# Performance work log

Measured on AMD Instinct MI355X. Metric: run time of the kernel, lower is better.

## Reference

```python
import jax, jax.numpy as jnp
import numpy as np

B, S, V, CTX, NC, D, NH, L, FF, MAXS = 8, 512, 32000, 8, 512, 256, 4, 4, 512, 512
PAD = 0  # ram_model.pad_token_id


def setup_inputs() -> dict:
    key = jax.random.key(0)
    ks = iter(jax.random.split(key, 64))
    def p(shape, s=0.02):
        return jax.random.normal(next(ks), shape, jnp.float32) * s
    inp = {}
    inp["token_ids"] = jax.random.randint(next(ks), (B, S), 0, V)
    inp["ram_table"] = p((V, NC), 0.1)          # frozen RAM per-cluster scores
    inp["proj_W"] = p((NC, D)); inp["proj_b"] = jnp.zeros((D,), jnp.float32)
    inp["pos_emb"] = p((MAXS, D))
    for pre in ("sa", "ca"):
        for nm in ("Wq", "Wk", "Wv", "Wo"):
            inp[f"{pre}_{nm}"] = p((L, D, D))
        for nm in ("bq", "bk", "bv", "bo"):
            inp[f"{pre}_{nm}"] = jnp.zeros((L, D), jnp.float32)
    for i in (1, 2, 3):
        inp[f"ln{i}_s"] = jnp.ones((L, D), jnp.float32)
        inp[f"ln{i}_b"] = jnp.zeros((L, D), jnp.float32)
    inp["ff_W1"] = p((L, D, FF)); inp["ff_b1"] = jnp.zeros((L, FF), jnp.float32)
    inp["ff_W2"] = p((L, FF, D)); inp["ff_b2"] = jnp.zeros((L, D), jnp.float32)
    inp["out_W"] = p((D, V)); inp["out_b"] = jnp.zeros((V,), jnp.float32)
    return inp


def _ln(x, s, b):
    m = x.mean(-1, keepdims=True)
    v = ((x - m) ** 2).mean(-1, keepdims=True)
    return (x - m) * jax.lax.rsqrt(v + 1e-5) * s + b


def _mha(q_in, k_in, v_in, Wq, bq, Wk, bk, Wv, bv, Wo, bo, mask):
    b, sq, d = q_in.shape
    hd = d // NH
    q = (q_in @ Wq + bq).reshape(b, sq, NH, hd)
    k = (k_in @ Wk + bk).reshape(b, -1, NH, hd)
    v = (v_in @ Wv + bv).reshape(b, -1, NH, hd)
    sc = jnp.einsum("bqhd,bkhd->bhqk", q, k) / np.sqrt(hd).astype(np.float32)
    if mask is not None:
        sc = jnp.where(mask, -1e9, sc)  # mask broadcast over [b, h]
    a = jax.nn.softmax(sc, axis=-1)
    o = jnp.einsum("bhqk,bkhd->bqhd", a, v).reshape(b, sq, d)
    return o @ Wo + bo


def _forward(token_ids, ram_table, proj_W, proj_b, pos_emb,
             sa_Wq, sa_bq, sa_Wk, sa_bk, sa_Wv, sa_bv, sa_Wo, sa_bo,
             ca_Wq, ca_bq, ca_Wk, ca_bk, ca_Wv, ca_bv, ca_Wo, ca_bo,
             ln1_s, ln1_b, ln2_s, ln2_b, ln3_s, ln3_b,
             ff_W1, ff_b1, ff_W2, ff_b2, out_W, out_b):
    b, s = token_ids.shape
    # Batched sliding context windows (replaces the per-position Python loop):
    # left-pad with PAD so window at pos covers [pos-CTX+1, pos].
    padded = jnp.concatenate(
        [jnp.full((b, CTX - 1), PAD, token_ids.dtype), token_ids], axis=1)
    idx = jnp.arange(s)[:, None] + jnp.arange(CTX)[None, :]  # [S, CTX]
    win = padded[:, idx]                                      # [B, S, CTX]
    # Frozen RAM feature extraction: per-cluster scores averaged over window.
    scores = ram_table[win].mean(axis=2)                      # [B, S, NC]
    x = scores @ proj_W + proj_b + pos_emb[:s]                # [B, S, D]
    mask = jnp.triu(jnp.ones((s, s), bool), 1)                # causal
    mem = jnp.zeros((b, 1, D), x.dtype)
    for l in range(L):
        h = _ln(x, ln1_s[l], ln1_b[l])
        x = x + _mha(h, h, h, sa_Wq[l], sa_bq[l], sa_Wk[l], sa_bk[l],
                     sa_Wv[l], sa_bv[l], sa_Wo[l], sa_bo[l], mask)
        h = _ln(x, ln2_s[l], ln2_b[l])
        x = x + _mha(h, mem, mem, ca_Wq[l], ca_bq[l], ca_Wk[l], ca_bk[l],
                     ca_Wv[l], ca_bv[l], ca_Wo[l], ca_bo[l], None)
        h = _ln(x, ln3_s[l], ln3_b[l])
        x = x + jax.nn.relu(h @ ff_W1[l] + ff_b1[l]) @ ff_W2[l] + ff_b2[l]
    return x @ out_W + out_b                                  # [B, S, V]


def reference(token_ids, ram_table, proj_W, proj_b, pos_emb,
              sa_Wq, sa_bq, sa_Wk, sa_bk, sa_Wv, sa_bv, sa_Wo, sa_bo,
              ca_Wq, ca_bq, ca_Wk, ca_bk, ca_Wv, ca_bv, ca_Wo, ca_bo,
              ln1_s, ln1_b, ln2_s, ln2_b, ln3_s, ln3_b,
              ff_W1, ff_b1, ff_W2, ff_b2, out_W, out_b):
    return _forward(token_ids, ram_table, proj_W, proj_b, pos_emb,
                    sa_Wq, sa_bq, sa_Wk, sa_bk, sa_Wv, sa_bv, sa_Wo, sa_bo,
                    ca_Wq, ca_bq, ca_Wk, ca_bk, ca_Wv, ca_bv, ca_Wo, ca_bo,
                    ln1_s, ln1_b, ln2_s, ln2_b, ln3_s, ln3_b,
                    ff_W1, ff_b1, ff_W2, ff_b2, out_W, out_b)
```

## Files before the change

### kernel.cpp

```cpp
#include <hip/hip_runtime.h>

#define B_   8
#define S_   512
#define V_   32000
#define CTX_ 8
#define NC_  512
#define D_   256
#define NH_  4
#define L_   4
#define FF_  512
#define HD_  64
#define BS_  4096

#define FG_F32   1
#define FG_BF16  2
#define FG_RELU  4
#define FG_POS   8
#define FG_NT    16
#define FG_QKV   32

typedef __attribute__((ext_vector_type(8))) short bf16x8;
typedef __attribute__((ext_vector_type(4))) float f32x4;

__device__ inline void gload16(const void* g, void* lds) {
    __builtin_amdgcn_global_load_lds(
        (const __attribute__((address_space(1))) void*)g,
        (__attribute__((address_space(3))) void*)lds, 16, 0, 0);
}

__device__ inline ushort f2b(float f) {
    union { float f; unsigned u; } v; v.f = f;
    unsigned u = v.u;
    unsigned r = u + 0x7fffu + ((u >> 16) & 1u);
    return (ushort)(r >> 16);
}

__global__ __launch_bounds__(256) void prologue_kernel(
    const int* __restrict__ tok, const float* __restrict__ ram,
    const float* __restrict__ proj_W, const float* __restrict__ Wq,
    const float* __restrict__ Wk, const float* __restrict__ Wv,
    const float* __restrict__ Wo, const float* __restrict__ W1,
    const float* __restrict__ W2, const float* __restrict__ outW,
    const float* __restrict__ ca_bv, const float* __restrict__ ca_Wo,
    const float* __restrict__ ca_bo, const float* __restrict__ bq,
    const float* __restrict__ bk, const float* __restrict__ bv,
    ushort* __restrict__ pjWb, ushort* __restrict__ WqkvB,
    ushort* __restrict__ WoB, ushort* __restrict__ ff1B,
    ushort* __restrict__ ff2B, ushort* __restrict__ Wb,
    float* __restrict__ cc, float* __restrict__ qkvb,
    ushort* __restrict__ scores)
{
    __shared__ float tile[32 * 33];
    int id = blockIdx.x;
    int t = threadIdx.x;
    if (id < 10176) {
        const float* src; ushort* dst; int K, N, lt;
        if (id < 128)       { src = proj_W; dst = pjWb; K = 512; N = 256; lt = id; }
        else if (id < 896)  { lt = id - 128; int z = lt >> 6; lt &= 63;
                              int which = z / L_, l = z % L_;
                              src = (which == 0 ? Wq : which == 1 ? Wk : Wv) + (size_t)l * 65536;
                              dst = WqkvB + ((size_t)l * 768 + which * 256) * 256;
                              K = 256; N = 256; }
        else if (id < 1152) { lt = id - 896; int l = lt >> 6; lt &= 63;
                              src = Wo + (size_t)l * 65536; dst = WoB + (size_t)l * 65536;
                              K = 256; N = 256; }
        else if (id < 1664) { lt = id - 1152; int l = lt >> 7; lt &= 127;
                              src = W1 + (size_t)l * 131072; dst = ff1B + (size_t)l * 131072;
                              K = 256; N = 512; }
        else if (id < 2176) { lt = id - 1664; int l = lt >> 7; lt &= 127;
                              src = W2 + (size_t)l * 131072; dst = ff2B + (size_t)l * 131072;
                              K = 512; N = 256; }
        else                { lt = id - 2176; src = outW; dst = Wb; K = 256; N = 32000; }
        int ntc = N >> 5;
        int n0 = (lt % ntc) * 32, k0 = (lt / ntc) * 32;
        int tx = t & 31, ty = t >> 5;
        for (int i = ty; i < 32; i += 8)
            tile[i * 33 + tx] = src[(size_t)(k0 + i) * N + n0 + tx];
        __syncthreads();
        for (int i = ty; i < 32; i += 8)
            dst[(size_t)(n0 + i) * K + k0 + tx] = f2b(tile[tx * 33 + i]);
    } else if (id < 10180) {
        int l = id - 10176;
        const float* w = ca_Wo + (size_t)l * D_ * D_;
        const float* b = ca_bv + l * D_;
        float acc = 0.f;
        for (int d = 0; d < D_; ++d) acc += b[d] * w[(size_t)d * D_ + t];
        cc[l * D_ + t] = acc + ca_bo[l * D_ + t];
        for (int u = t; u < 768; u += 256) {
            int which = u >> 8, c = u & 255;
            const float* src = which == 0 ? bq : which == 1 ? bk : bv;
            qkvb[l * 768 + u] = src[l * 256 + c];
        }
    } else {
        int bs = id - 10180;
        int b = bs >> 9, s = bs & 511;
        float a0 = 0.f, a1 = 0.f;
        #pragma unroll
        for (int c = 0; c < CTX_; ++c) {
            int pos = s + c - (CTX_ - 1);
            int tk = (pos < 0) ? 0 : tok[b * S_ + pos];
            const float* row = ram + (size_t)tk * NC_;
            a0 += row[t];
            a1 += row[t + 256];
        }
        scores[(size_t)bs * NC_ + t]       = f2b(a0 * 0.125f);
        scores[(size_t)bs * NC_ + t + 256] = f2b(a1 * 0.125f);
    }
}

template<int K, int FLAGS>
__global__ __launch_bounds__(256) void gemm_row(
    const ushort* __restrict__ A, const ushort* __restrict__ Bt,
    const float* __restrict__ bias, const float* __restrict__ extra,
    const float* __restrict__ resid, const float* __restrict__ pos,
    const float* __restrict__ lnS, const float* __restrict__ lnB,
    float* __restrict__ Xout, ushort* __restrict__ Hout)
{
    __shared__ ushort As[16 * 64];
    __shared__ ushort Bs[256 * 64];
    __shared__ float red[2][4][16];
    int mt = blockIdx.x;
    int row0 = mt * 16;
    int t = threadIdx.x, w = t >> 6, lane = t & 63;
    int srow = lane >> 3, slot = lane & 7;
    int gcol = (slot ^ srow) * 8;
    int sl = lane >> 4, lc = lane & 15;
    int rA = lane & 15;

    f32x4 acc[4] = {};

    #pragma unroll
    for (int k0 = 0; k0 < K; k0 += 64) {
        if (w < 2)
            gload16(A + (size_t)(row0 + w * 8 + srow) * K + k0 + gcol, As + w * 512);
        #pragma unroll
        for (int c = 0; c < 8; ++c) {
            int chunk = w * 8 + c;
            gload16(Bt + (size_t)(chunk * 8 + srow) * K + k0 + gcol, Bs + chunk * 512);
        }
        __syncthreads();
        #pragma unroll
        for (int kk = 0; kk < 2; ++kk) {
            bf16x8 a = *reinterpret_cast<const bf16x8*>(
                As + rA * 64 + (((sl + kk * 4) ^ (rA & 7)) * 8));
            #pragma unroll
            for (int n = 0; n < 4; ++n) {
                int rr = w * 64 + (lane & 15) + n * 16;
                bf16x8 b = *reinterpret_cast<const bf16x8*>(
                    Bs + rr * 64 + (((sl + kk * 4) ^ (rr & 7)) * 8));
                acc[n] = __builtin_amdgcn_mfma_f32_16x16x32_bf16(a, b, acc[n], 0, 0, 0);
            }
        }
        __syncthreads();
    }

    float v[4][4];
    float psum[4] = {}, psq[4] = {};
    #pragma unroll
    for (int n = 0; n < 4; ++n) {
        int col = w * 64 + n * 16 + lc;
        float bn = bias[col];
        float en = extra ? extra[col] : 0.f;
        #pragma unroll
        for (int r = 0; r < 4; ++r) {
            int row = row0 + sl * 4 + r;
            float x = acc[n][r] + bn;
            if constexpr (FLAGS & FG_POS) x += pos[(size_t)(row & 511) * D_ + col];
            x += en;
            if (resid) x += resid[(size_t)row * D_ + col];
            v[n][r] = x;
            psum[r] += x;
            psq[r] += x * x;
        }
    }
    #pragma unroll
    for (int r = 0; r < 4; ++r) {
        #pragma unroll
        for (int o = 8; o > 0; o >>= 1) {
            psum[r] += __shfl_xor(psum[r], o);
            psq[r]  += __shfl_xor(psq[r], o);
        }
    }
    if (lc == 0) {
        #pragma unroll
        for (int r = 0; r < 4; ++r) {
            red[0][w][sl * 4 + r] = psum[r];
            red[1][w][sl * 4 + r] = psq[r];
        }
    }
    __syncthreads();
    #pragma unroll
    for (int r = 0; r < 4; ++r) {
        int rl = sl * 4 + r;
        float s  = red[0][0][rl] + red[0][1][rl] + red[0][2][rl] + red[0][3][rl];
        float s2 = red[1][0][rl] + red[1][1][rl] + red[1][2][rl] + red[1][3][rl];
        float mean = s * (1.f / D_);
        float var = s2 * (1.f / D_) - mean * mean;
        float rstd = rsqrtf(var + 1e-5f);
        int row = row0 + rl;
        #pragma unroll
        for (int n = 0; n < 4; ++n) {
            int col = w * 64 + n * 16 + lc;
            float x = v[n][r];
            Xout[(size_t)row * D_ + col] = x;
            Hout[(size_t)row * D_ + col] =
                f2b((x - mean) * rstd * lnS[col] + lnB[col]);
        }
    }
}

template<bool LAST>
__global__ __launch_bounds__(256) void tail_fused_kernel(
    const ushort* __restrict__ pv, const ushort* __restrict__ WoT,
    const float* __restrict__ bo, const float* __restrict__ ccl,
    const float* __restrict__ xin,
    const float* __restrict__ ln3S, const float* __restrict__ ln3B,
    const ushort* __restrict__ W1t, const ushort* __restrict__ W2t,
    const float* __restrict__ b1, const float* __restrict__ b2,
    const float* __restrict__ ln1S, const float* __restrict__ ln1B,
    float* __restrict__ Xout, ushort* __restrict__ Hout,
    ushort* __restrict__ XBout)
{
    __shared__ ushort Ah[16 * 256];
    __shared__ ushort As1[16 * 64];
    __shared__ ushort Bs1[64 * 256];
    __shared__ ushort Bs2[256 * 64];
    __shared__ ushort As2[16 * 64];
    __shared__ float red[2][4][16];
    int row0 = blockIdx.x * 16;
    int t = threadIdx.x, w = t >> 6, lane = t & 63;
    int srow = lane >> 3, slot = lane & 7;
    int gcol = (slot ^ srow) * 8;
    int sl = lane >> 4, lc = lane & 15;
    int rA = lane & 15;

    f32x4 acc[4] = {};
    #pragma unroll
    for (int k0 = 0; k0 < 256; k0 += 64) {
        if (w < 2)
            gload16(pv + (size_t)(row0 + w * 8 + srow) * 256 + k0 + gcol, As1 + w * 512);
        #pragma unroll
        for (int c = 0; c < 8; ++c) {
            int chunk = w * 8 + c;
            gload16(WoT + (size_t)(chunk * 8 + srow) * 256 + k0 + gcol, Bs2 + chunk * 512);
        }
        __syncthreads();
        #pragma unroll
        for (int kk = 0; kk < 2; ++kk) {
            bf16x8 a = *reinterpret_cast<const bf16x8*>(
                As1 + rA * 64 + (((sl + kk * 4) ^ (rA & 7)) * 8));
            #pragma unroll
            for (int n = 0; n < 4; ++n) {
                int rr = w * 64 + rA + n * 16;
                bf16x8 b = *reinterpret_cast<const bf16x8*>(
                    Bs2 + rr * 64 + (((sl + kk * 4) ^ (rr & 7)) * 8));
                acc[n] = __builtin_amdgcn_mfma_f32_16x16x32_bf16(a, b, acc[n], 0, 0, 0);
            }
        }
        __syncthreads();
    }

    float v[4][4];
    {
        float psum[4] = {}, psq[4] = {};
        #pragma unroll
        for (int n = 0; n < 4; ++n) {
            int col = w * 64 + n * 16 + lc;
            float bn = bo[col] + ccl[col];
            #pragma unroll
            for (int r = 0; r < 4; ++r) {
                int row = row0 + sl * 4 + r;
                float x = acc[n][r] + bn + xin[(size_t)row * D_ + col];
                v[n][r] = x;
                psum[r] += x;
                psq[r] += x * x;
            }
        }
        #pragma unroll
        for (int r = 0; r < 4; ++r) {
            #pragma unroll
            for (int o = 8; o > 0; o >>= 1) {
                psum[r] += __shfl_xor(psum[r], o);
                psq[r]  += __shfl_xor(psq[r], o);
            }
        }
        if (lc == 0) {
            #pragma unroll
            for (int r = 0; r < 4; ++r) {
                red[0][w][sl * 4 + r] = psum[r];
                red[1][w][sl * 4 + r] = psq[r];
            }
        }
        __syncthreads();
        #pragma unroll
        for (int r = 0; r < 4; ++r) {
            int rl = sl * 4 + r;
            float s  = red[0][0][rl] + red[0][1][rl] + red[0][2][rl] + red[0][3][rl];
            float s2 = red[1][0][rl] + red[1][1][rl] + red[1][2][rl] + red[1][3][rl];
            float mean = s * (1.f / D_);
            float var = s2 * (1.f / D_) - mean * mean;
            float rstd = rsqrtf(var + 1e-5f);
            #pragma unroll
            for (int n = 0; n < 4; ++n) {
                int col = w * 64 + n * 16 + lc;
                int colk = n * 16 + lc;
                float h = (v[n][r] - mean) * rstd * ln3S[col] + ln3B[col];
                Ah[w * 1024 + rl * 64 + (((colk >> 3) ^ (rl & 7)) * 8) + (colk & 7)] =
                    f2b(h);
            }
        }
    }
    __syncthreads();

    f32x4 xacc[4] = {};
    for (int c8 = 0; c8 < 8; ++c8) {
        int f0 = c8 * 64;
        #pragma unroll
        for (int c = 0; c < 8; ++c) {
            int chunk = w * 8 + c;
            int ks = chunk >> 3, rg = chunk & 7;
            gload16(W1t + (size_t)(f0 + rg * 8 + srow) * 256 + ks * 64 + gcol,
                    Bs1 + chunk * 512);
        }
        #pragma unroll
        for (int c = 0; c < 8; ++c) {
            int chunk = w * 8 + c;
            gload16(W2t + (size_t)(chunk * 8 + srow) * 512 + f0 + gcol,
                    Bs2 + chunk * 512);
        }
        __syncthreads();

        f32x4 a2 = {};
        #pragma unroll
        for (int ks = 0; ks < 4; ++ks) {
            #pragma unroll
            for (int kk = 0; kk < 2; ++kk) {
                bf16x8 a = *reinterpret_cast<const bf16x8*>(
                    Ah + ks * 1024 + rA * 64 + (((sl + kk * 4) ^ (rA & 7)) * 8));
                int rB = w * 16 + rA;
                bf16x8 b = *reinterpret_cast<const bf16x8*>(
                    Bs1 + ks * 4096 + rB * 64 + (((sl + kk * 4) ^ (rB & 7)) * 8));
                a2 = __builtin_amdgcn_mfma_f32_16x16x32_bf16(a, b, a2, 0, 0, 0);
            }
        }
        {
            float bn = b1[f0 + w * 16 + lc];
            #pragma unroll
            for (int r = 0; r < 4; ++r) {
                float p = fmaxf(a2[r] + bn, 0.f);
                int prow = sl * 4 + r;
                int pcol = w * 16 + lc;
                As2[prow * 64 + (((pcol >> 3) ^ (prow & 7)) * 8) + (pcol & 7)] = f2b(p);
            }
        }
        __syncthreads();
        #pragma unroll
        for (int kk = 0; kk < 2; ++kk) {
            bf16x8 a = *reinterpret_cast<const bf16x8*>(
                As2 + rA * 64 + (((sl + kk * 4) ^ (rA & 7)) * 8));
            #pragma unroll
            for (int n = 0; n < 4; ++n) {
                int rB = w * 64 + n * 16 + rA;
                bf16x8 b = *reinterpret_cast<const bf16x8*>(
                    Bs2 + rB * 64 + (((sl + kk * 4) ^ (rB & 7)) * 8));
                xacc[n] = __builtin_amdgcn_mfma_f32_16x16x32_bf16(a, b, xacc[n], 0, 0, 0);
            }
        }
        __syncthreads();
    }

    float psum[4] = {}, psq[4] = {};
    #pragma unroll
    for (int n = 0; n < 4; ++n) {
        int col = w * 64 + n * 16 + lc;
        float bn = b2[col];
        #pragma unroll
        for (int r = 0; r < 4; ++r) {
            float x = xacc[n][r] + bn + v[n][r];
            v[n][r] = x;
            psum[r] += x;
            psq[r] += x * x;
        }
    }
    if constexpr (LAST) {
        #pragma unroll
        for (int n = 0; n < 4; ++n) {
            int col = w * 64 + n * 16 + lc;
            #pragma unroll
            for (int r = 0; r < 4; ++r) {
                int row = row0 + sl * 4 + r;
                XBout[(size_t)row * D_ + col] = f2b(v[n][r]);
            }
        }
        return;
    }
    #pragma unroll
    for (int r = 0; r < 4; ++r) {
        #pragma unroll
        for (int o = 8; o > 0; o >>= 1) {
            psum[r] += __shfl_xor(psum[r], o);
            psq[r]  += __shfl_xor(psq[r], o);
        }
    }
    if (lc == 0) {
        #pragma unroll
        for (int r = 0; r < 4; ++r) {
            red[0][w][sl * 4 + r] = psum[r];
            red[1][w][sl * 4 + r] = psq[r];
        }
    }
    __syncthreads();
    #pragma unroll
    for (int r = 0; r < 4; ++r) {
        int rl = sl * 4 + r;
        float s  = red[0][0][rl] + red[0][1][rl] + red[0][2][rl] + red[0][3][rl];
        float s2 = red[1][0][rl] + red[1][1][rl] + red[1][2][rl] + red[1][3][rl];
        float mean = s * (1.f / D_);
        float var = s2 * (1.f / D_) - mean * mean;
        float rstd = rsqrtf(var + 1e-5f);
        int row = row0 + rl;
        #pragma unroll
        for (int n = 0; n < 4; ++n) {
            int col = w * 64 + n * 16 + lc;
            float x = v[n][r];
            Xout[(size_t)row * D_ + col] = x;
            Hout[(size_t)row * D_ + col] =
                f2b((x - mean) * rstd * ln1S[col] + ln1B[col]);
        }
    }
}

template<int BM, int BN, int K, int TN, int FLAGS>
__global__ __launch_bounds__(256) void gemm_t(
    const ushort* __restrict__ A, const ushort* __restrict__ Bt,
    const float* __restrict__ bias, const float* __restrict__ extra,
    const float* __restrict__ resid, const float* __restrict__ pos,
    float* __restrict__ Cf, ushort* __restrict__ Cb)
{
    constexpr int WM = BM / 32;
    constexpr int WN = BN / 32;
    constexpr int MT = 4096 / BM;
    constexpr int NWG = MT * (TN / BN);
    __shared__ ushort smem[(BM + BN) * 64];
    ushort* As = smem;
    ushort* Bs = smem + BM * 64;
    int bid = blockIdx.x;
    int swz = bid;
    if constexpr ((NWG & 7) == 0) {
        constexpr int cpx = NWG >> 3;
        swz = (bid & 7) * cpx + (bid >> 3);
    }
    int mt = swz % MT, nt = swz / MT;
    int row0 = mt * BM, col0 = nt * BN;
    int t = threadIdx.x, w = t >> 6, lane = t & 63;
    int wr = w >> 1, wc = w & 1;
    int srow = lane >> 3, slot = lane & 7;
    int gcol = (slot ^ srow) * 8;

    f32x4 acc[WM][WN] = {};
    int sl = lane >> 4;
    int rA0 = wr * (BM / 2) + (lane & 15);
    int rB0 = wc * (BN / 2) + (lane & 15);

    #pragma unroll
    for (int k0 = 0; k0 < K; k0 += 64) {
        #pragma unroll
        for (int c = 0; c < BM / 32; ++c) {
            int chunk = w * (BM / 32) + c;
            gload16(A + (size_t)(row0 + chunk * 8 + srow) * K + k0 + gcol,
                    As + chunk * 512);
        }
        #pragma unroll
        for (int c = 0; c < BN / 32; ++c) {
            int chunk = w * (BN / 32) + c;
            gload16(Bt + (size_t)(col0 + chunk * 8 + srow) * K + k0 + gcol,
                    Bs + chunk * 512);
        }
        __syncthreads();
        #pragma unroll
        for (int kk = 0; kk < 2; ++kk) {
            bf16x8 a[WM], b[WN];
            #pragma unroll
            for (int m = 0; m < WM; ++m) {
                int rr = rA0 + m * 16;
                a[m] = *reinterpret_cast<const bf16x8*>(
                    As + rr * 64 + (((sl + kk * 4) ^ (rr & 7)) * 8));
            }
            #pragma unroll
            for (int n = 0; n < WN; ++n) {
                int rr = rB0 + n * 16;
                b[n] = *reinterpret_cast<const bf16x8*>(
                    Bs + rr * 64 + (((sl + kk * 4) ^ (rr & 7)) * 8));
            }
            #pragma unroll
            for (int m = 0; m < WM; ++m)
                #pragma unroll
                for (int n = 0; n < WN; ++n)
                    acc[m][n] = __builtin_amdgcn_mfma_f32_16x16x32_bf16(
                        a[m], b[n], acc[m][n], 0, 0, 0);
        }
        __syncthreads();
    }

    int lr = (lane >> 4) * 4;
    int lc = lane & 15;

    if constexpr (FLAGS & FG_NT) {
        float* Ct = reinterpret_cast<float*>(smem);
        #pragma unroll
        for (int p = 0; p < 2; ++p) {
            __syncthreads();
            if (wr == p) {
                #pragma unroll
                for (int n = 0; n < WN; ++n) {
                    int colL = wc * (BN / 2) + n * 16 + lc;
                    float bn = bias[col0 + colL];
                    #pragma unroll
                    for (int m = 0; m < WM; ++m)
                        #pragma unroll
                        for (int r = 0; r < 4; ++r)
                            Ct[(m * 16 + lr + r) * BN + colL] = acc[m][n][r] + bn;
                }
            }
            __syncthreads();
            constexpr int NV4 = (BM / 2) * (BN / 4);
            #pragma unroll
            for (int j = 0; j < NV4 / 256; ++j) {
                int idx = t + j * 256;
                int rl = idx / (BN / 4);
                int c4 = idx % (BN / 4);
                f32x4 v4 = reinterpret_cast<const f32x4*>(Ct)[idx];
                __builtin_nontemporal_store(v4,
                    reinterpret_cast<f32x4*>(
                        &Cf[(size_t)(row0 + p * (BM / 2) + rl) * TN + col0 + c4 * 4]));
            }
        }
        return;
    }

    #pragma unroll
    for (int n = 0; n < WN; ++n) {
        int col = col0 + wc * (BN / 2) + n * 16 + lc;
        float bn = bias ? bias[col] : 0.f;
        float en = extra ? extra[col] : 0.f;
        #pragma unroll
        for (int m = 0; m < WM; ++m) {
            int rbase = row0 + wr * (BM / 2) + m * 16 + lr;
            #pragma unroll
            for (int r = 0; r < 4; ++r) {
                int row = rbase + r;
                float v = acc[m][n][r] + bn;
                if constexpr (FLAGS & FG_QKV) {
                    int which = col >> 8;
                    int c2 = col & 255;
                    int hh = c2 >> 6, dd = c2 & 63;
                    int bb = row >> 9, ss = row & 511;
                    if (which == 0) {
                        Cb[((((size_t)bb * NH_ + hh) * S_ + ss) << 6) + dd] =
                            f2b(v * 0.125f);
                    } else if (which == 1) {
                        (Cb + 1048576)[((((size_t)bb * NH_ + hh) * S_ + ss) << 6) + dd] =
                            f2b(v);
                    } else {
                        (Cb + 2097152)[((((size_t)bb * NH_ + hh) * HD_ + dd) << 9) + ss] =
                            f2b(v);
                    }
                } else {
                    if constexpr (FLAGS & FG_POS) v += pos[(size_t)(row & 511) * TN + col];
                    if (extra) v += en;
                    if (resid) v += resid[(size_t)row * TN + col];
                    if constexpr (FLAGS & FG_RELU) v = fmaxf(v, 0.f);
                    if constexpr (FLAGS & FG_BF16)
                        Cb[(size_t)row * TN + col] = f2b(v);
                    if constexpr (FLAGS & FG_F32)
                        Cf[(size_t)row * TN + col] = v;
                }
            }
        }
    }
}

__global__ __launch_bounds__(256) void attn_kernel(
    const ushort* __restrict__ q, const ushort* __restrict__ k,
    const ushort* __restrict__ vT, ushort* __restrict__ pv)
{
    int qt = blockIdx.x, bh = blockIdx.y;
    __shared__ ushort smem[20480];
    ushort* Ps = smem + 16384;
    int t = threadIdx.x, w = t >> 6, lane = t & 63;
    int srow = lane >> 3, slot = lane & 7;
    int gcol = (slot ^ srow) * 8;
    int sl = lane >> 4, lc = lane & 15;

    const ushort* Qp = q + ((size_t)bh * S_ + qt * 64) * HD_;
    const ushort* Kp = k + (size_t)bh * S_ * HD_;
    const ushort* Vp = vT + (size_t)bh * HD_ * S_;

    int qrow = w * 16 + lc;
    bf16x8 qf0 = *reinterpret_cast<const bf16x8*>(Qp + qrow * 64 + sl * 8);
    bf16x8 qf1 = *reinterpret_cast<const bf16x8*>(Qp + qrow * 64 + sl * 8 + 32);

    f32x4 o[4] = {};
    float m_r[4], l_r[4];
    #pragma unroll
    for (int r = 0; r < 4; ++r) { m_r[r] = -1e30f; l_r[r] = 0.f; }
    int row_abs = qt * 64 + w * 16 + sl * 4;

    {
        ushort* Ks = smem;
        ushort* Vs = smem + 4096;
        #pragma unroll
        for (int c = 0; c < 2; ++c) {
            int chunk = w * 2 + c;
            gload16(Kp + (size_t)(chunk * 8 + srow) * 64 + gcol, Ks + chunk * 512);
            gload16(Vp + (size_t)(chunk * 8 + srow) * 512 + gcol, Vs + chunk * 512);
        }
    }

    for (int kt = 0; kt <= qt; ++kt) {
        int cur = kt & 1;
        ushort* Ks = smem + cur * 8192;
        ushort* Vs = smem + cur * 8192 + 4096;
        __syncthreads();
        if (kt < qt) {
            ushort* Kn = smem + (cur ^ 1) * 8192;
            ushort* Vn = Kn + 4096;
            #pragma unroll
            for (int c = 0; c < 2; ++c) {
                int chunk = w * 2 + c;
                gload16(Kp + (size_t)((kt + 1) * 64 + chunk * 8 + srow) * 64 + gcol,
                        Kn + chunk * 512);
                gload16(Vp + (size_t)(chunk * 8 + srow) * 512 + (kt + 1) * 64 + gcol,
                        Vn + chunk * 512);
            }
        }

        f32x4 sa[4] = {};
        #pragma unroll
        for (int n = 0; n < 4; ++n) {
            int rB = n * 16 + lc;
            bf16x8 b0 = *reinterpret_cast<const bf16x8*>(
                Ks + rB * 64 + ((sl ^ (rB & 7)) * 8));
            bf16x8 b1 = *reinterpret_cast<const bf16x8*>(
                Ks + rB * 64 + (((sl + 4) ^ (rB & 7)) * 8));
            sa[n] = __builtin_amdgcn_mfma_f32_16x16x32_bf16(qf0, b0, sa[n], 0, 0, 0);
            sa[n] = __builtin_amdgcn_mfma_f32_16x16x32_bf16(qf1, b1, sa[n], 0, 0, 0);
        }
        if (kt == qt) {
            #pragma unroll
            for (int n = 0; n < 4; ++n) {
                int col = kt * 64 + n * 16 + lc;
                #pragma unroll
                for (int r = 0; r < 4; ++r)
                    if (col > row_abs + r) sa[n][r] = -1e30f;
            }
        }
        float psum[4];
        #pragma unroll
        for (int r = 0; r < 4; ++r) {
            float vm = fmaxf(fmaxf(sa[0][r], sa[1][r]), fmaxf(sa[2][r], sa[3][r]));
            vm = fmaxf(vm, __shfl_xor(vm, 1));
            vm = fmaxf(vm, __shfl_xor(vm, 2));
            vm = fmaxf(vm, __shfl_xor(vm, 4));
            vm = fmaxf(vm, __shfl_xor(vm, 8));
            float mn = fmaxf(m_r[r], vm);
            float scl = __expf(m_r[r] - mn);
            m_r[r] = mn;
            l_r[r] *= scl;
            #pragma unroll
            for (int n = 0; n < 4; ++n) o[n][r] *= scl;
            psum[r] = 0.f;
        }
        ushort* Pw = Ps + w * 1024;
        #pragma unroll
        for (int n = 0; n < 4; ++n) {
            #pragma unroll
            for (int r = 0; r < 4; ++r) {
                float p = __expf(sa[n][r] - m_r[r]);
                psum[r] += p;
                int prow = sl * 4 + r;
                int pcol = n * 16 + lc;
                int pslot = pcol >> 3;
                Pw[prow * 64 + ((pslot ^ (prow & 7)) * 8) + (pcol & 7)] = f2b(p);
            }
        }
        #pragma unroll
        for (int r = 0; r < 4; ++r) {
            float s = psum[r];
            s += __shfl_xor(s, 1);
            s += __shfl_xor(s, 2);
            s += __shfl_xor(s, 4);
            s += __shfl_xor(s, 8);
            l_r[r] += s;
        }
        int arow = lc;
        bf16x8 pa0 = *reinterpret_cast<const bf16x8*>(
            Pw + arow * 64 + ((sl ^ (arow & 7)) * 8));
        bf16x8 pa1 = *reinterpret_cast<const bf16x8*>(
            Pw + arow * 64 + (((sl + 4) ^ (arow & 7)) * 8));
        #pragma unroll
        for (int n = 0; n < 4; ++n) {
            int rB = n * 16 + lc;
            bf16x8 v0 = *reinterpret_cast<const bf16x8*>(
                Vs + rB * 64 + ((sl ^ (rB & 7)) * 8));
            bf16x8 v1 = *reinterpret_cast<const bf16x8*>(
                Vs + rB * 64 + (((sl + 4) ^ (rB & 7)) * 8));
            o[n] = __builtin_amdgcn_mfma_f32_16x16x32_bf16(pa0, v0, o[n], 0, 0, 0);
            o[n] = __builtin_amdgcn_mfma_f32_16x16x32_bf16(pa1, v1, o[n], 0, 0, 0);
        }
    }

    int bb = bh >> 2, hh = bh & 3;
    #pragma unroll
    for (int r = 0; r < 4; ++r) {
        float inv = 1.f / l_r[r];
        int ss = qt * 64 + w * 16 + sl * 4 + r;
        #pragma unroll
        for (int n = 0; n < 4; ++n) {
            int dd = n * 16 + lc;
            pv[((size_t)bb * S_ + ss) * D_ + hh * HD_ + dd] = f2b(o[n][r] * inv);
        }
    }
}

extern "C" void kernel_launch(void* const* d_in, const int* in_sizes, int n_in,
                              void* d_out, int out_size, void* d_ws, size_t ws_size,
                              hipStream_t stream)
{
    const int*   tok     = (const int*)  d_in[0];
    const float* ram     = (const float*)d_in[1];
    const float* proj_W  = (const float*)d_in[2];
    const float* proj_b  = (const float*)d_in[3];
    const float* pos_emb = (const float*)d_in[4];
    const float* sa_Wq   = (const float*)d_in[5];
    const float* sa_Wk   = (const float*)d_in[6];
    const float* sa_Wv   = (const float*)d_in[7];
    const float* sa_Wo   = (const float*)d_in[8];
    const float* sa_bq   = (const float*)d_in[9];
    const float* sa_bk   = (const float*)d_in[10];
    const float* sa_bv   = (const float*)d_in[11];
    const float* sa_bo   = (const float*)d_in[12];
    const float* ca_Wo   = (const float*)d_in[16];
    const float* ca_bv   = (const float*)d_in[19];
    const float* ca_bo   = (const float*)d_in[20];
    const float* ln1_s   = (const float*)d_in[21];
    const float* ln1_b   = (const float*)d_in[22];
    const float* ln3_s   = (const float*)d_in[25];
    const float* ln3_b   = (const float*)d_in[26];
    const float* ff_W1   = (const float*)d_in[27];
    const float* ff_b1   = (const float*)d_in[28];
    const float* ff_W2   = (const float*)d_in[29];
    const float* ff_b2   = (const float*)d_in[30];
    const float* out_W   = (const float*)d_in[31];
    const float* out_b   = (const float*)d_in[32];

    float* out = (float*)d_out;
    float* ws  = (float*)d_ws;

    float*  x   = ws;
    float*  cc  = ws + (size_t)BS_ * D_;
    ushort* xb  = (ushort*)(cc + L_ * D_);
    ushort* Wb  = xb + (size_t)BS_ * D_;

    ushort* sc_b  = (ushort*)out;
    ushort* h_b   = sc_b + 2097152;
    ushort* qkv3  = h_b + 1048576;
    ushort* pv_b  = qkv3 + 3145728;
    ushort* pjWb  = pv_b + 1048576;
    ushort* WqkvB = pjWb + 131072;
    ushort* WoB   = WqkvB + 786432;
    ushort* ff1B  = WoB + 262144;
    ushort* ff2B  = ff1B + 524288;
    float*  qkvb  = (float*)(ff2B + 524288);
    ushort* qb_b  = qkv3;
    ushort* kb_b  = qkv3 + 1048576;
    ushort* vT_b  = qkv3 + 2097152;

    prologue_kernel<<<14276, 256, 0, stream>>>(
        tok, ram, proj_W, sa_Wq, sa_Wk, sa_Wv, sa_Wo, ff_W1, ff_W2, out_W,
        ca_bv, ca_Wo, ca_bo, sa_bq, sa_bk, sa_bv,
        pjWb, WqkvB, WoB, ff1B, ff2B, Wb, cc, qkvb, sc_b);

    gemm_row<512, FG_POS><<<256, 256, 0, stream>>>(
        sc_b, pjWb, proj_b, nullptr, nullptr, pos_emb,
        ln1_s, ln1_b, x, h_b);

    for (int l = 0; l < L_; ++l) {
        gemm_t<64, 64, 256, 768, FG_QKV><<<768, 256, 0, stream>>>(
            h_b, WqkvB + (size_t)l * 196608, qkvb + l * 768,
            nullptr, nullptr, nullptr, nullptr, qkv3);
        attn_kernel<<<dim3(8, 32), 256, 0, stream>>>(qb_b, kb_b, vT_b, pv_b);
        if (l < L_ - 1) {
            tail_fused_kernel<false><<<256, 256, 0, stream>>>(
                pv_b, WoB + (size_t)l * 65536, sa_bo + l * D_, cc + l * D_, x,
                ln3_s + l * D_, ln3_b + l * D_,
                ff1B + (size_t)l * 131072, ff2B + (size_t)l * 131072,
                ff_b1 + l * FF_, ff_b2 + l * D_,
                ln1_s + (l + 1) * D_, ln1_b + (l + 1) * D_, x, h_b, nullptr);
        } else {
            tail_fused_kernel<true><<<256, 256, 0, stream>>>(
                pv_b, WoB + (size_t)l * 65536, sa_bo + l * D_, cc + l * D_, x,
                ln3_s + l * D_, ln3_b + l * D_,
                ff1B + (size_t)l * 131072, ff2B + (size_t)l * 131072,
                ff_b1 + l * FF_, ff_b2 + l * D_,
                nullptr, nullptr, nullptr, nullptr, xb);
        }
    }

    gemm_t<128, 128, 256, 32000, FG_F32 | FG_NT><<<8000, 256, 0, stream>>>(
        xb, Wb, out_b, nullptr, nullptr, nullptr, out, nullptr);
}
```

Baseline: 350.4 us.

## Fuse QKV projection into preceding LayerNorm row kernels

Result: slower. 369.4 us (+5.4%).

```diff
diff --git a/kernel.cpp b/kernel.cpp
--- a/kernel.cpp
+++ b/kernel.cpp
@@ -33,6 +33,60 @@
     unsigned u = v.u;
     unsigned r = u + 0x7fffu + ((u >> 16) & 1u);
     return (ushort)(r >> 16);
+}
+
+__device__ __forceinline__ void qkv_phase(
+    const ushort* Ah, ushort* Bsb, const ushort* __restrict__ Wqkv,
+    const float* __restrict__ qb, ushort* __restrict__ qkv3,
+    int row0, int t)
+{
+    int w = t >> 6, lane = t & 63;
+    int srow = lane >> 3, slot = lane & 7;
+    int gcol = (slot ^ srow) * 8;
+    int sl = lane >> 4, lc = lane & 15;
+    int rA = lane & 15;
+    for (int c12 = 0; c12 < 12; ++c12) {
+        int f0 = c12 * 64;
+        #pragma unroll
+        for (int c = 0; c < 8; ++c) {
+            int chunk = w * 8 + c;
+            int ks = chunk >> 3, rg = chunk & 7;
+            gload16(Wqkv + (size_t)(f0 + rg * 8 + srow) * 256 + ks * 64 + gcol,
+                    Bsb + chunk * 512);
+        }
+        __syncthreads();
+        f32x4 a2 = {};
+        #pragma unroll
+        for (int ks = 0; ks < 4; ++ks) {
+            #pragma unroll
+            for (int kk = 0; kk < 2; ++kk) {
+                bf16x8 a = *reinterpret_cast<const bf16x8*>(
+                    Ah + ks * 1024 + rA * 64 + (((sl + kk * 4) ^ (rA & 7)) * 8));
+                int rB = w * 16 + rA;
+                bf16x8 b = *reinterpret_cast<const bf16x8*>(
+                    Bsb + ks * 4096 + rB * 64 + (((sl + kk * 4) ^ (rB & 7)) * 8));
+                a2 = __builtin_amdgcn_mfma_f32_16x16x32_bf16(a, b, a2, 0, 0, 0);
+            }
+        }
+        int col = f0 + w * 16 + lc;
+        float bn = qb[col];
+        int which = col >> 8;
+        int c2 = col & 255;
+        int hh = c2 >> 6, dd = c2 & 63;
+        #pragma unroll
+        for (int r = 0; r < 4; ++r) {
+            int row = row0 + sl * 4 + r;
+            int bb = row >> 9, ss = row & 511;
+            float v = a2[r] + bn;
+            if (which == 0)
+                qkv3[((((size_t)bb * NH_ + hh) * S_ + ss) << 6) + dd] = f2b(v * 0.125f);
+            else if (which == 1)
+                (qkv3 + 1048576)[((((size_t)bb * NH_ + hh) * S_ + ss) << 6) + dd] = f2b(v);
+            else
+                (qkv3 + 2097152)[((((size_t)bb * NH_ + hh) * HD_ + dd) << 9) + ss] = f2b(v);
+        }
+        __syncthreads();
+    }
 }
 
 __global__ __launch_bounds__(256) void prologue_kernel(
@@ -111,13 +165,14 @@
 template<int K, int FLAGS>
 __global__ __launch_bounds__(256) void gemm_row(
     const ushort* __restrict__ A, const ushort* __restrict__ Bt,
-    const float* __restrict__ bias, const float* __restrict__ extra,
-    const float* __restrict__ resid, const float* __restrict__ pos,
+    const float* __restrict__ bias, const float* __restrict__ pos,
     const float* __restrict__ lnS, const float* __restrict__ lnB,
-    float* __restrict__ Xout, ushort* __restrict__ Hout)
+    const ushort* __restrict__ Wqkv, const float* __restrict__ qb,
+    float* __restrict__ Xout, ushort* __restrict__ qkv3)
 {
     __shared__ ushort As[16 * 64];
     __shared__ ushort Bs[256 * 64];
+    __shared__ ushort Ah[16 * 256];
     __shared__ float red[2][4][16];
     int mt = blockIdx.x;
     int row0 = mt * 16;
@@ -145,7 +200,7 @@
                 As + rA * 64 + (((sl + kk * 4) ^ (rA & 7)) * 8));
             #pragma unroll
             for (int n = 0; n < 4; ++n) {
-                int rr = w * 64 + (lane & 15) + n * 16;
+                int rr = w * 64 + rA + n * 16;
                 bf16x8 b = *reinterpret_cast<const bf16x8*>(
                     Bs + rr * 64 + (((sl + kk * 4) ^ (rr & 7)) * 8));
                 acc[n] = __builtin_amdgcn_mfma_f32_16x16x32_bf16(a, b, acc[n], 0, 0, 0);
@@ -160,14 +215,11 @@
     for (int n = 0; n < 4; ++n) {
         int col = w * 64 + n * 16 + lc;
         float bn = bias[col];
-        float en = extra ? extra[col] : 0.f;
         #pragma unroll
         for (int r = 0; r < 4; ++r) {
             int row = row0 + sl * 4 + r;
             float x = acc[n][r] + bn;
             if constexpr (FLAGS & FG_POS) x += pos[(size_t)(row & 511) * D_ + col];
-            x += en;
-            if (resid) x += resid[(size_t)row * D_ + col];
             v[n][r] = x;
             psum[r] += x;
             psq[r] += x * x;
@@ -201,12 +253,14 @@
         #pragma unroll
         for (int n = 0; n < 4; ++n) {
             int col = w * 64 + n * 16 + lc;
+            int colk = n * 16 + lc;
             float x = v[n][r];
             Xout[(size_t)row * D_ + col] = x;
-            Hout[(size_t)row * D_ + col] =
+            Ah[w * 1024 + rl * 64 + (((colk >> 3) ^ (rl & 7)) * 8) + (colk & 7)] =
                 f2b((x - mean) * rstd * lnS[col] + lnB[col]);
         }
     }
+    qkv_phase(Ah, Bs, Wqkv, qb, qkv3, row0, t);
 }
 
 template<bool LAST>
@@ -218,7 +272,8 @@
     const ushort* __restrict__ W1t, const ushort* __restrict__ W2t,
     const float* __restrict__ b1, const float* __restrict__ b2,
     const float* __restrict__ ln1S, const float* __restrict__ ln1B,
-    float* __restrict__ Xout, ushort* __restrict__ Hout,
+    const ushort* __restrict__ WqkvN, const float* __restrict__ qbN,
+    float* __restrict__ Xout, ushort* __restrict__ qkv3,
     ushort* __restrict__ XBout)
 {
     __shared__ ushort Ah[16 * 256];
@@ -422,20 +477,21 @@
         #pragma unroll
         for (int n = 0; n < 4; ++n) {
             int col = w * 64 + n * 16 + lc;
+            int colk = n * 16 + lc;
             float x = v[n][r];
             Xout[(size_t)row * D_ + col] = x;
-            Hout[(size_t)row * D_ + col] =
+            Ah[w * 1024 + rl * 64 + (((colk >> 3) ^ (rl & 7)) * 8) + (colk & 7)] =
                 f2b((x - mean) * rstd * ln1S[col] + ln1B[col]);
         }
     }
+    __syncthreads();
+    qkv_phase(Ah, Bs1, WqkvN, qbN, qkv3, row0, t);
 }
 
 template<int BM, int BN, int K, int TN, int FLAGS>
 __global__ __launch_bounds__(256) void gemm_t(
     const ushort* __restrict__ A, const ushort* __restrict__ Bt,
-    const float* __restrict__ bias, const float* __restrict__ extra,
-    const float* __restrict__ resid, const float* __restrict__ pos,
-    float* __restrict__ Cf, ushort* __restrict__ Cb)
+    const float* __restrict__ bias, float* __restrict__ Cf)
 {
     constexpr int WM = BM / 32;
     constexpr int WN = BN / 32;
@@ -504,78 +560,33 @@
 
     int lr = (lane >> 4) * 4;
     int lc = lane & 15;
-
-    if constexpr (FLAGS & FG_NT) {
-        float* Ct = reinterpret_cast<float*>(smem);
-        #pragma unroll
-        for (int p = 0; p < 2; ++p) {
-            __syncthreads();
-            if (wr == p) {
+    float* Ct = reinterpret_cast<float*>(smem);
+    #pragma unroll
+    for (int p = 0; p < 2; ++p) {
+        __syncthreads();
+        if (wr == p) {
+            #pragma unroll
+            for (int n = 0; n < WN; ++n) {
+                int colL = wc * (BN / 2) + n * 16 + lc;
+                float bn = bias[col0 + colL];
                 #pragma unroll
-                for (int n = 0; n < WN; ++n) {
-                    int colL = wc * (BN / 2) + n * 16 + lc;
-                    float bn = bias[col0 + colL];
+                for (int m = 0; m < WM; ++m)
                     #pragma unroll
-                    for (int m = 0; m < WM; ++m)
-                        #pragma unroll
-                        for (int r = 0; r < 4; ++r)
-                            Ct[(m * 16 + lr + r) * BN + colL] = acc[m][n][r] + bn;
-                }
-            }
-            __syncthreads();
-            constexpr int NV4 = (BM / 2) * (BN / 4);
-            #pragma unroll
-            for (int j = 0; j < NV4 / 256; ++j) {
-                int idx = t + j * 256;
-                int rl = idx / (BN / 4);
-                int c4 = idx % (BN / 4);
-                f32x4 v4 = reinterpret_cast<const f32x4*>(Ct)[idx];
-                __builtin_nontemporal_store(v4,
-                    reinterpret_cast<f32x4*>(
-                        &Cf[(size_t)(row0 + p * (BM / 2) + rl) * TN + col0 + c4 * 4]));
-            }
-        }
-        return;
-    }
-
-    #pragma unroll
-    for (int n = 0; n < WN; ++n) {
-        int col = col0 + wc * (BN / 2) + n * 16 + lc;
-        float bn = bias ? bias[col] : 0.f;
-        float en = extra ? extra[col] : 0.f;
-        #pragma unroll
-        for (int m = 0; m < WM; ++m) {
-            int rbase = row0 + wr * (BM / 2) + m * 16 + lr;
-            #pragma unroll
-            for (int r = 0; r < 4; ++r) {
-                int row = rbase + r;
-                float v = acc[m][n][r] + bn;
-                if constexpr (FLAGS & FG_QKV) {
-                    int which = col >> 8;
-                    int c2 = col & 255;
-                    int hh = c2 >> 6, dd = c2 & 63;
-                    int bb = row >> 9, ss = row & 511;
-                    if (which == 0) {
-                        Cb[((((size_t)bb * NH_ + hh) * S_ + ss) << 6) + dd] =
-                            f2b(v * 0.125f);
-                    } else if (which == 1) {
-                        (Cb + 1048576)[((((size_t)bb * NH_ + hh) * S_ + ss) << 6) + dd] =
-                            f2b(v);
-                    } else {
-                        (Cb + 2097152)[((((size_t)bb * NH_ + hh) * HD_ + dd) << 9) + ss] =
-                            f2b(v);
-                    }
-                } else {
-                    if constexpr (FLAGS & FG_POS) v += pos[(size_t)(row & 511) * TN + col];
-                    if (extra) v += en;
-                    if (resid) v += resid[(size_t)row * TN + col];
-                    if constexpr (FLAGS & FG_RELU) v = fmaxf(v, 0.f);
-                    if constexpr (FLAGS & FG_BF16)
-                        Cb[(size_t)row * TN + col] = f2b(v);
-                    if constexpr (FLAGS & FG_F32)
-                        Cf[(size_t)row * TN + col] = v;
-                }
-            }
+                    for (int r = 0; r < 4; ++r)
+                        Ct[(m * 16 + lr + r) * BN + colL] = acc[m][n][r] + bn;
+            }
+        }
+        __syncthreads();
+        constexpr int NV4 = (BM / 2) * (BN / 4);
+        #pragma unroll
+        for (int j = 0; j < NV4 / 256; ++j) {
+            int idx = t + j * 256;
+            int rl = idx / (BN / 4);
+            int c4 = idx % (BN / 4);
+            f32x4 v4 = reinterpret_cast<const f32x4*>(Ct)[idx];
+            __builtin_nontemporal_store(v4,
+                reinterpret_cast<f32x4*>(
+                    &Cf[(size_t)(row0 + p * (BM / 2) + rl) * TN + col0 + c4 * 4]));
         }
     }
 }
@@ -763,8 +774,7 @@
     ushort* Wb  = xb + (size_t)BS_ * D_;
 
     ushort* sc_b  = (ushort*)out;
-    ushort* h_b   = sc_b + 2097152;
-    ushort* qkv3  = h_b + 1048576;
+    ushort* qkv3  = sc_b + 2097152;
     ushort* pv_b  = qkv3 + 3145728;
     ushort* pjWb  = pv_b + 1048576;
     ushort* WqkvB = pjWb + 131072;
@@ -782,13 +792,10 @@
         pjWb, WqkvB, WoB, ff1B, ff2B, Wb, cc, qkvb, sc_b);
 
     gemm_row<512, FG_POS><<<256, 256, 0, stream>>>(
-        sc_b, pjWb, proj_b, nullptr, nullptr, pos_emb,
-        ln1_s, ln1_b, x, h_b);
+        sc_b, pjWb, proj_b, pos_emb, ln1_s, ln1_b,
+        WqkvB, qkvb, x, qkv3);
 
     for (int l = 0; l < L_; ++l) {
-        gemm_t<64, 64, 256, 768, FG_QKV><<<768, 256, 0, stream>>>(
-            h_b, WqkvB + (size_t)l * 196608, qkvb + l * 768,
-            nullptr, nullptr, nullptr, nullptr, qkv3);
         attn_kernel<<<dim3(8, 32), 256, 0, stream>>>(qb_b, kb_b, vT_b, pv_b);
         if (l < L_ - 1) {
             tail_fused_kernel<false><<<256, 256, 0, stream>>>(
@@ -796,17 +803,20 @@
                 ln3_s + l * D_, ln3_b + l * D_,
                 ff1B + (size_t)l * 131072, ff2B + (size_t)l * 131072,
                 ff_b1 + l * FF_, ff_b2 + l * D_,
-                ln1_s + (l + 1) * D_, ln1_b + (l + 1) * D_, x, h_b, nullptr);
+                ln1_s + (l + 1) * D_, ln1_b + (l + 1) * D_,
+                WqkvB + (size_t)(l + 1) * 196608, qkvb + (l + 1) * 768,
+                x, qkv3, nullptr);
         } else {
             tail_fused_kernel<true><<<256, 256, 0, stream>>>(
                 pv_b, WoB + (size_t)l * 65536, sa_bo + l * D_, cc + l * D_, x,
                 ln3_s + l * D_, ln3_b + l * D_,
                 ff1B + (size_t)l * 131072, ff2B + (size_t)l * 131072,
                 ff_b1 + l * FF_, ff_b2 + l * D_,
-                nullptr, nullptr, nullptr, nullptr, xb);
-        }
-    }
-
-    gemm_t<128, 128, 256, 32000, FG_F32 | FG_NT><<<8000, 256, 0, stream>>>(
-        xb, Wb, out_b, nullptr, nullptr, nullptr, out, nullptr);
+                nullptr, nullptr, nullptr, nullptr,
+                x, nullptr, xb);
+        }
+    }
+
+    gemm_t<128, 128, 256, 32000, FG_NT><<<8000, 256, 0, stream>>>(
+        xb, Wb, out_b, out);
 }
```
